# Kernel tuning notes

Hardware: AMD Instinct MI355X
Metric: run time of the kernel (lower is better)

Reference implementation:

```python
import jax, jax.numpy as jnp
import numpy as np

MARGIN = 0.2
LAMBDA_SOFTMAX = 9.0
LAMBDA_LSE = 6.0
WEIGHT_FACTOR = 0.7  # attn_prev is absent/zero on the i2t path
EPS = 1e-8
NEG_INF = -1e9


def setup_inputs() -> dict:
    key = jax.random.key(0)
    k1, k2, k3 = jax.random.split(key, 3)
    B, R, W, D = 128, 36, 32, 256  # batch, regions, max words, feat dim
    im = jax.random.normal(k1, (B, R, D), jnp.float32)
    s = jax.random.normal(k2, (B, W, D), jnp.float32)
    s_l = jax.random.randint(k3, (B,), 1, W + 1)  # caption lengths in [1, W]
    return {"im": im, "s": s, "s_l": s_l}


def _xattn_scores_i2t(im, s, s_l):
    # im: (B, R, D) images; s: (C, W, D) captions; s_l: (C,) lengths
    C, W = s.shape[0], s.shape[1]
    word_mask = jnp.arange(W)[None, :] < s_l[:, None]  # (C, W)

    # func_attention(query=images, context=caption words):
    # attn[c,b,w,r] = <s[c,w], im[b,r]>
    attn = jnp.einsum('cwd,brd->cbwr', s, im)
    # raw_feature_norm == 'clipped_l2norm': LeakyReLU(0.1) then l2norm over region axis
    attn = jax.nn.leaky_relu(attn, 0.1)
    attn = attn / (jnp.sqrt(jnp.sum(attn * attn, axis=-1, keepdims=True)) + EPS)
    # softmax over sourceL = words, with smoothing; mask padded words
    logits = jnp.where(word_mask[:, None, :, None], attn * LAMBDA_SOFTMAX, NEG_INF)
    A = jax.nn.softmax(logits, axis=2)  # (C, B, W, R), sums to 1 over words
    # weightedContext[c,b,r,:] = 0.7 * sum_w A[c,b,w,r] * s[c,w,:]
    wC = WEIGHT_FACTOR * jnp.einsum('cbwr,cwd->cbrd', A, s)

    # cosine similarity between image regions and weighted caption context
    num = jnp.sum(im[None] * wC, axis=-1)                      # (C, B, R)
    denom = jnp.linalg.norm(im, axis=-1)[None] * jnp.linalg.norm(wC, axis=-1)
    row_sim = num / jnp.clip(denom, EPS)

    # agg_func == 'LogSumExp' over regions
    sim = jax.nn.logsumexp(LAMBDA_LSE * row_sim, axis=2) / LAMBDA_LSE  # (C, B)
    return sim.T  # scores: (n_image, n_caption)


def reference(im, s, s_l):
    scores = _xattn_scores_i2t(im, s, s_l)
    diag = jnp.diag(scores)
    cost_s = jnp.clip(MARGIN + scores - diag[:, None], 0.0)   # caption retrieval
    cost_im = jnp.clip(MARGIN + scores - diag[None, :], 0.0)  # image retrieval
    eye = jnp.eye(scores.shape[0], dtype=bool)
    cost_s = jnp.where(eye, 0.0, cost_s)
    cost_im = jnp.where(eye, 0.0, cost_im)
    # max_violation=True: hardest negatives
    return jnp.sum(jnp.max(cost_s, axis=1)) + jnp.sum(jnp.max(cost_im, axis=0))
```

## Files before the change

### kernel.cpp

```cpp
#include <hip/hip_runtime.h>
#include <math.h>

#define CN 128
#define RN 36
#define WN 32
#define DN 256

#define SSTR  264
#define GSTR  40
#define ATSTR 40

#define WS_SCORES 0
#define WS_SF   65536
#define WS_IMF  (WS_SF + CN*16384)
#define WS_TAIL (WS_IMF + CN*16384)
#define WS_N2I  (WS_TAIL + CN*2048)
#define WS_NEED (WS_N2I + CN*RN*4)

typedef unsigned short u16;
typedef __attribute__((ext_vector_type(4))) unsigned short u16x4;
typedef __attribute__((ext_vector_type(8))) unsigned short u16x8;
typedef __attribute__((ext_vector_type(8))) __bf16 bf16x8;
typedef __attribute__((ext_vector_type(4))) float f32x4;

#define C9   12.9842502f
#define C6   8.65616798f
#define IC6  0.115524530f

__device__ __forceinline__ float bf2f(u16 u){ return __uint_as_float(((unsigned)u)<<16); }
__device__ __forceinline__ u16 f2bf(float f){ unsigned x=__float_as_uint(f); return (u16)((x + 0x7fffu + ((x>>16)&1u))>>16); }
__device__ __forceinline__ u16 f2bf_hw(float f){ __bf16 h = (__bf16)f; return __builtin_bit_cast(u16, h); }
__device__ __forceinline__ float lrelu(float v){ return fmaxf(v, 0.1f*v); }

__device__ __forceinline__ void gload16(const void* g, void* l){
    __builtin_amdgcn_global_load_lds((const __attribute__((address_space(1))) void*)g,
                                     (__attribute__((address_space(3))) void*)l, 16, 0, 0);
}

__global__ __launch_bounds__(256)
void precompute_kernel(const float* __restrict__ im, const float* __restrict__ s,
                       char* __restrict__ ws)
{
    const int tid = threadIdx.x;
    if (blockIdx.x < 128) {
        const int i = blockIdx.x;
        const float* src = s + (size_t)i*(WN*DN);
        u16* out = (u16*)(ws + WS_SF) + (size_t)i*8192;
#pragma unroll
        for (int it = 0; it < 4; it++) {
            int idx = tid + it*256;
            int m = idx >> 9, ks = (idx >> 6) & 7, ln = idx & 63;
            int col = ln & 15, g4 = ln >> 4;
            const float4* p = (const float4*)(src + (m*16+col)*DN + ks*32 + g4*8);
            float4 v0 = p[0], v1 = p[1];
            u16x8 hh = { f2bf_hw(v0.x),f2bf_hw(v0.y),f2bf_hw(v0.z),f2bf_hw(v0.w),
                         f2bf_hw(v1.x),f2bf_hw(v1.y),f2bf_hw(v1.z),f2bf_hw(v1.w) };
            *(u16x8*)(out + (size_t)idx*8) = hh;
        }
    } else {
        const int i = blockIdx.x - 128;
        const float* src = im + (size_t)i*(RN*DN);
        u16* out = (u16*)(ws + WS_IMF) + (size_t)i*8192;
#pragma unroll
        for (int it = 0; it < 4; it++) {
            int idx = tid + it*256;
            int m = idx >> 9, ks = (idx >> 6) & 7, ln = idx & 63;
            int col = ln & 15, g4 = ln >> 4;
            const float4* p = (const float4*)(src + (m*16+col)*DN + ks*32 + g4*8);
            float4 v0 = p[0], v1 = p[1];
            u16x8 hh = { f2bf_hw(v0.x),f2bf_hw(v0.y),f2bf_hw(v0.z),f2bf_hw(v0.w),
                         f2bf_hw(v1.x),f2bf_hw(v1.y),f2bf_hw(v1.z),f2bf_hw(v1.w) };
            *(u16x8*)(out + (size_t)idx*8) = hh;
        }
        if (tid < 128) {
            int row = tid >> 5, x = tid & 31;
            const float4* p = (const float4*)(src + (32+row)*DN + x*8);
            float4 v0 = p[0], v1 = p[1];
            u16x8 hh = { f2bf_hw(v0.x),f2bf_hw(v0.y),f2bf_hw(v0.z),f2bf_hw(v0.w),
                         f2bf_hw(v1.x),f2bf_hw(v1.y),f2bf_hw(v1.z),f2bf_hw(v1.w) };
            *(u16x8*)((u16*)(ws + WS_TAIL) + (size_t)i*1024 + row*256 + x*8) = hh;
        }
        float* n2o = (float*)(ws + WS_N2I) + (size_t)i*RN;
#pragma unroll
        for (int it = 0; it < 2; it++) {
            int idx = tid + it*256;
            if (idx < 288) {
                int r = idx >> 3, q = idx & 7;
                const float4* p = (const float4*)(src + r*DN + q*32);
                float ss = 0.f;
#pragma unroll
                for (int k = 0; k < 8; k++) {
                    float4 v = p[k];
                    ss = fmaf(v.x,v.x,ss); ss = fmaf(v.y,v.y,ss);
                    ss = fmaf(v.z,v.z,ss); ss = fmaf(v.w,v.w,ss);
                }
                ss += __shfl_xor(ss,1); ss += __shfl_xor(ss,2); ss += __shfl_xor(ss,4);
                if (q == 0) n2o[r] = ss;
            }
        }
    }
}

__global__ __launch_bounds__(512, 3)
void xattn_staged(const int* __restrict__ s_l, char* __restrict__ ws)
{
    __shared__ __align__(16) u16 smem[22016];
    u16* lds_g = smem + 4096;

    const int tid = threadIdx.x;
    const int lane = tid & 63, wv = tid >> 6;
    const int bq = blockIdx.x, cp = blockIdx.y;
    const int ci = wv >> 2, bi = wv & 3;
    const int c = cp*2 + ci, b = bq*4 + bi;
    const int col = lane & 15, g4 = lane >> 4;
    const int gm = bi >> 1, gn = bi & 1;
    const int L = s_l[c];
    const int r2c = (32+col > 35) ? 35 : 32+col;
    const int trow = (col > 3) ? 3 : col;

    {
        const char* tsrc = ws + WS_TAIL + (size_t)(bq*4)*2048;
        gload16(tsrc + wv*1024 + lane*16, (char*)smem + wv*1024);
    }
    const float* n2p = (const float*)(ws + WS_N2I) + (size_t)b*RN;
    float n2v0 = n2p[col];
    float n2v1 = n2p[16+col];
    float n2v2 = n2p[r2c];
    __syncthreads();

    const char* sf = ws + WS_SF  + (size_t)c*16384;
    const char* mf = ws + WS_IMF + (size_t)b*16384;
    const u16*  tl = smem + bi*1024;

    f32x4 raw[2][3];
#pragma unroll
    for (int m = 0; m < 2; m++)
#pragma unroll
        for (int n = 0; n < 3; n++) raw[m][n] = (f32x4){0.f,0.f,0.f,0.f};
    f32x4 gacc = {0.f,0.f,0.f,0.f};

#pragma unroll
    for (int ks = 0; ks < 8; ks++) {
        bf16x8 a0 = *(const bf16x8*)(sf +        ks*1024 + lane*16);
        bf16x8 a1 = *(const bf16x8*)(sf + 8192 + ks*1024 + lane*16);
        bf16x8 b0 = *(const bf16x8*)(mf +        ks*1024 + lane*16);
        bf16x8 b1 = *(const bf16x8*)(mf + 8192 + ks*1024 + lane*16);
        bf16x8 b2 = *(const bf16x8*)&tl[trow*256 + ks*32 + g4*8];
        bf16x8 ga = gm ? a1 : a0;
        bf16x8 gb = gn ? a1 : a0;
        raw[0][0] = __builtin_amdgcn_mfma_f32_16x16x32_bf16(a0, b0, raw[0][0], 0,0,0);
        raw[0][1] = __builtin_amdgcn_mfma_f32_16x16x32_bf16(a0, b1, raw[0][1], 0,0,0);
        raw[0][2] = __builtin_amdgcn_mfma_f32_16x16x32_bf16(a0, b2, raw[0][2], 0,0,0);
        raw[1][0] = __builtin_amdgcn_mfma_f32_16x16x32_bf16(a1, b0, raw[1][0], 0,0,0);
        raw[1][1] = __builtin_amdgcn_mfma_f32_16x16x32_bf16(a1, b1, raw[1][1], 0,0,0);
        raw[1][2] = __builtin_amdgcn_mfma_f32_16x16x32_bf16(a1, b2, raw[1][2], 0,0,0);
        gacc      = __builtin_amdgcn_mfma_f32_16x16x32_bf16(ga, gb, gacc, 0,0,0);
    }

    {
        u16x4 hg = { f2bf_hw(gacc[0]), f2bf_hw(gacc[1]), f2bf_hw(gacc[2]), f2bf_hw(gacc[3]) };
        *(u16x4*)&lds_g[ci*1280 + (gn*16+col)*GSTR + gm*16 + g4*4] = hg;
    }

    float af[2][3][4];
#pragma unroll
    for (int m = 0; m < 2; m++) {
#pragma unroll
        for (int reg = 0; reg < 4; reg++) {
            float ssum = 0.f;
#pragma unroll
            for (int n = 0; n < 3; n++) {
                float v = lrelu(raw[m][n][reg]);
                if (n == 2 && col >= 4) v = 0.f;
                af[m][n][reg] = v;
                ssum = fmaf(v, v, ssum);
            }
            ssum += __shfl_xor(ssum, 1);
            ssum += __shfl_xor(ssum, 2);
            ssum += __shfl_xor(ssum, 4);
            ssum += __shfl_xor(ssum, 8);
            float inv2 = C9 / (sqrtf(ssum) + 1e-8f);
#pragma unroll
            for (int n = 0; n < 3; n++) af[m][n][reg] *= inv2;
        }
    }

    float num[3];
#pragma unroll
    for (int n = 0; n < 3; n++) {
        float nm = 0.f;
#pragma unroll
        for (int m = 0; m < 2; m++)
#pragma unroll
            for (int reg = 0; reg < 4; reg++) {
                int w = m*16 + g4*4 + reg;
                float e = (w < L) ? __builtin_amdgcn_exp2f(af[m][n][reg]) : 0.f;
                af[m][n][reg] = e;
                nm = fmaf(e, raw[m][n][reg], nm);
            }
        nm += __shfl_xor(nm, 16);
        nm += __shfl_xor(nm, 32);
        num[n] = nm;
    }

    __syncthreads();

    u16* at = smem + 6656 + wv*1920;
#pragma unroll
    for (int m = 0; m < 2; m++)
#pragma unroll
        for (int n = 0; n < 3; n++) {
            u16x4 h = { f2bf_hw(af[m][n][0]), f2bf_hw(af[m][n][1]),
                        f2bf_hw(af[m][n][2]), f2bf_hw(af[m][n][3]) };
            *(u16x4*)&at[(n*16 + col)*ATSTR + m*16 + g4*4] = h;
        }

    bf16x8 gf0 = *(const bf16x8*)&lds_g[ci*1280 + col*GSTR + g4*8];
    bf16x8 gf1 = *(const bf16x8*)&lds_g[ci*1280 + (16+col)*GSTR + g4*8];

    float qv[3];
#pragma unroll
    for (int n = 0; n < 3; n++) {
        bf16x8 bfv = *(const bf16x8*)&at[(n*16 + col)*ATSTR + g4*8];
        f32x4 z = {0.f,0.f,0.f,0.f};
        f32x4 t0 = __builtin_amdgcn_mfma_f32_16x16x32_bf16(gf0, bfv, z, 0,0,0);
        f32x4 t1 = __builtin_amdgcn_mfma_f32_16x16x32_bf16(gf1, bfv, z, 0,0,0);
        float q = 0.f;
#pragma unroll
        for (int reg = 0; reg < 4; reg++) {
            q = fmaf(af[0][n][reg], t0[reg], q);
            q = fmaf(af[1][n][reg], t1[reg], q);
        }
        q += __shfl_xor(q, 16);
        q += __shfl_xor(q, 32);
        qv[n] = q;
    }

    float es = 0.f;
#pragma unroll
    for (int n = 0; n < 3; n++) {
        float n2a = (n == 0) ? n2v0 : (n == 1) ? n2v1 : n2v2;
        float rs = num[n] * rsqrtf(fmaxf(n2a * qv[n], 1e-16f));
        bool valid = (n < 2) || (col < 4);
        if (valid) es += __builtin_amdgcn_exp2f(C6 * rs);
    }
    es += __shfl_xor(es, 1);
    es += __shfl_xor(es, 2);
    es += __shfl_xor(es, 4);
    es += __shfl_xor(es, 8);

    if (lane == 0)
        ((float*)(ws + WS_SCORES))[(size_t)b * CN + c] =
            __builtin_amdgcn_logf(es) * IC6;
}

__global__ __launch_bounds__(512, 2)
void xattn_fallback(const float* __restrict__ im, const float* __restrict__ s,
                    const int* __restrict__ s_l, float* __restrict__ scores)
{
    __shared__ u16   s_lds[2][WN*SSTR];
    __shared__ u16   im_lds[4][RN*SSTR];
    __shared__ u16   g_lds[2][WN*GSTR];
    __shared__ u16   at_lds[8][48*ATSTR];
    __shared__ float n2i_lds[4][RN];

    const int tid  = threadIdx.x;
    const int lane = tid & 63;
    const int wv   = tid >> 6;
    const int bq   = blockIdx.x, cp = blockIdx.y;
    const int ci   = wv >> 2, bi = wv & 3;
    const int c    = cp*2 + ci, b = bq*4 + bi;
    const int col  = lane & 15, g4 = lane >> 4;

    if (wv < 4) {
        const float4* g = (const float4*)(im + (size_t)(bq*4 + wv) * (RN*DN));
        u16* dst = im_lds[wv];
#pragma unroll
        for (int k = 0; k < 36; k++) {
            int i = lane + k*64;
            float4 v = g[i];
            int row = i >> 6, cc = (i & 63) * 4;
            u16x4 h = { f2bf(v.x), f2bf(v.y), f2bf(v.z), f2bf(v.w) };
            *(u16x4*)&dst[row*SSTR + cc] = h;
        }
    } else {
        int cap = (wv - 4) >> 1;
        int l2  = ((wv - 4) & 1) * 64 + lane;
        const float4* g = (const float4*)(s + (size_t)(cp*2 + cap) * (WN*DN));
        u16* dst = s_lds[cap];
#pragma unroll
        for (int k = 0; k < 16; k++) {
            int i = l2 + k*128;
            float4 v = g[i];
            int row = i >> 6, cc = (i & 63) * 4;
            u16x4 h = { f2bf(v.x), f2bf(v.y), f2bf(v.z), f2bf(v.w) };
            *(u16x4*)&dst[row*SSTR + cc] = h;
        }
    }
    __syncthreads();

    {
        const int gm = (wv >> 1) & 1, gn = wv & 1;
        const u16* sb = s_lds[ci];
        f32x4 acc = {0.f, 0.f, 0.f, 0.f};
#pragma unroll
        for (int ks = 0; ks < 8; ks++) {
            int k0 = ks*32 + g4*8;
            bf16x8 af = *(const bf16x8*)&sb[(gm*16 + col)*SSTR + k0];
            bf16x8 bfv = *(const bf16x8*)&sb[(gn*16 + col)*SSTR + k0];
            acc = __builtin_amdgcn_mfma_f32_16x16x32_bf16(af, bfv, acc, 0, 0, 0);
        }
        u16x4 h = { f2bf(acc[0]), f2bf(acc[1]), f2bf(acc[2]), f2bf(acc[3]) };
        *(u16x4*)&g_lds[ci][(gn*16 + col)*GSTR + gm*16 + g4*4] = h;
    }

    if (wv < 4) {
        const u16* ib = im_lds[wv];
        int r = lane >> 1, half = lane & 1;
        float ss = 0.f;
        const u16x8* p = (const u16x8*)&ib[r*SSTR + half*128];
#pragma unroll
        for (int k = 0; k < 16; k++) {
            u16x8 v = p[k];
#pragma unroll
            for (int j = 0; j < 8; j++) { float f = bf2f(v[j]); ss = fmaf(f, f, ss); }
        }
        ss += __shfl_xor(ss, 1);
        if (half == 0) n2i_lds[wv][r] = ss;
        if (lane < 8) {
            int r2 = 32 + (lane >> 1), h2 = lane & 1;
            float s2 = 0.f;
            const u16x8* p2 = (const u16x8*)&ib[r2*SSTR + h2*128];
#pragma unroll
            for (int k = 0; k < 16; k++) {
                u16x8 v = p2[k];
#pragma unroll
                for (int j = 0; j < 8; j++) { float f = bf2f(v[j]); s2 = fmaf(f, f, s2); }
            }
            s2 += __shfl_xor(s2, 1);
            if (h2 == 0) n2i_lds[wv][r2] = s2;
        }
    }

    const u16* sb = s_lds[ci];
    const u16* ib = im_lds[bi];
    f32x4 raw[2][3];
#pragma unroll
    for (int m = 0; m < 2; m++)
#pragma unroll
        for (int n = 0; n < 3; n++) raw[m][n] = (f32x4){0.f,0.f,0.f,0.f};
    {
        int r2c = 32 + col; if (r2c > 35) r2c = 35;
#pragma unroll
        for (int ks = 0; ks < 8; ks++) {
            int k0 = ks*32 + g4*8;
            bf16x8 a0 = *(const bf16x8*)&sb[col*SSTR + k0];
            bf16x8 a1 = *(const bf16x8*)&sb[(16 + col)*SSTR + k0];
            bf16x8 b0 = *(const bf16x8*)&ib[col*SSTR + k0];
            bf16x8 b1 = *(const bf16x8*)&ib[(16 + col)*SSTR + k0];
            bf16x8 b2 = *(const bf16x8*)&ib[r2c*SSTR + k0];
            raw[0][0] = __builtin_amdgcn_mfma_f32_16x16x32_bf16(a0, b0, raw[0][0], 0,0,0);
            raw[0][1] = __builtin_amdgcn_mfma_f32_16x16x32_bf16(a0, b1, raw[0][1], 0,0,0);
            raw[0][2] = __builtin_amdgcn_mfma_f32_16x16x32_bf16(a0, b2, raw[0][2], 0,0,0);
            raw[1][0] = __builtin_amdgcn_mfma_f32_16x16x32_bf16(a1, b0, raw[1][0], 0,0,0);
            raw[1][1] = __builtin_amdgcn_mfma_f32_16x16x32_bf16(a1, b1, raw[1][1], 0,0,0);
            raw[1][2] = __builtin_amdgcn_mfma_f32_16x16x32_bf16(a1, b2, raw[1][2], 0,0,0);
        }
    }

    float af[2][3][4];
#pragma unroll
    for (int m = 0; m < 2; m++) {
#pragma unroll
        for (int reg = 0; reg < 4; reg++) {
            float ssum = 0.f;
#pragma unroll
            for (int n = 0; n < 3; n++) {
                float v = lrelu(raw[m][n][reg]);
                if (n == 2 && col >= 4) v = 0.f;
                af[m][n][reg] = v;
                ssum = fmaf(v, v, ssum);
            }
            ssum += __shfl_xor(ssum, 1);
            ssum += __shfl_xor(ssum, 2);
            ssum += __shfl_xor(ssum, 4);
            ssum += __shfl_xor(ssum, 8);
            float inv = 1.0f / (sqrtf(ssum) + 1e-8f);
#pragma unroll
            for (int n = 0; n < 3; n++) af[m][n][reg] *= inv;
        }
    }

    const int L = s_l[c];
    float num[3], qv[3];
#pragma unroll
    for (int n = 0; n < 3; n++) {
        float mx = -1e30f;
#pragma unroll
        for (int m = 0; m < 2; m++)
#pragma unroll
            for (int reg = 0; reg < 4; reg++) {
                int w = m*16 + g4*4 + reg;
                if (w < L) mx = fmaxf(mx, af[m][n][reg]);
            }
        mx = fmaxf(mx, __shfl_xor(mx, 16));
        mx = fmaxf(mx, __shfl_xor(mx, 32));
        mx *= 9.0f;
        float sme = 0.f;
#pragma unroll
        for (int m = 0; m < 2; m++)
#pragma unroll
            for (int reg = 0; reg < 4; reg++) {
                int w = m*16 + g4*4 + reg;
                float e = (w < L) ? __expf(fmaf(9.0f, af[m][n][reg], -mx)) : 0.f;
                af[m][n][reg] = e;
                sme += e;
            }
        sme += __shfl_xor(sme, 16);
        sme += __shfl_xor(sme, 32);
        float inv = 1.0f / sme;
        float nm = 0.f;
#pragma unroll
        for (int m = 0; m < 2; m++)
#pragma unroll
            for (int reg = 0; reg < 4; reg++) {
                af[m][n][reg] *= inv;
                nm = fmaf(af[m][n][reg], raw[m][n][reg], nm);
            }
        nm += __shfl_xor(nm, 16);
        nm += __shfl_xor(nm, 32);
        num[n] = nm;
    }

#pragma unroll
    for (int m = 0; m < 2; m++)
#pragma unroll
        for (int n = 0; n < 3; n++) {
            u16x4 h = { f2bf(af[m][n][0]), f2bf(af[m][n][1]),
                        f2bf(af[m][n][2]), f2bf(af[m][n][3]) };
            *(u16x4*)&at_lds[wv][(n*16 + col)*ATSTR + m*16 + g4*4] = h;
        }

    __syncthreads();

    bf16x8 gf0 = *(const bf16x8*)&g_lds[ci][col*GSTR + g4*8];
    bf16x8 gf1 = *(const bf16x8*)&g_lds[ci][(16+col)*GSTR + g4*8];
    f32x4 tt[2][3];
#pragma unroll
    for (int n = 0; n < 3; n++) {
        bf16x8 bfv = *(const bf16x8*)&at_lds[wv][(n*16 + col)*ATSTR + g4*8];
        f32x4 z = {0.f,0.f,0.f,0.f};
        tt[0][n] = __builtin_amdgcn_mfma_f32_16x16x32_bf16(gf0, bfv, z, 0,0,0);
        tt[1][n] = __builtin_amdgcn_mfma_f32_16x16x32_bf16(gf1, bfv, z, 0,0,0);
    }

#pragma unroll
    for (int n = 0; n < 3; n++) {
        float q = 0.f;
#pragma unroll
        for (int m = 0; m < 2; m++)
#pragma unroll
            for (int reg = 0; reg < 4; reg++) q = fmaf(af[m][n][reg], tt[m][n][reg], q);
        q += __shfl_xor(q, 16);
        q += __shfl_xor(q, 32);
        qv[n] = q;
    }

    float rs[3];
#pragma unroll
    for (int n = 0; n < 3; n++) {
        int r = n*16 + col; if (r > 35) r = 35;
        float n2 = n2i_lds[bi][r];
        float denom = fmaxf(0.7f * sqrtf(n2 * qv[n]), 1e-8f);
        rs[n] = 0.7f * num[n] / denom;
    }
    float xm = -1e30f;
#pragma unroll
    for (int n = 0; n < 3; n++) {
        bool valid = (n < 2) || (col < 4);
        if (valid) xm = fmaxf(xm, 6.0f * rs[n]);
    }
    xm = fmaxf(xm, __shfl_xor(xm, 1));
    xm = fmaxf(xm, __shfl_xor(xm, 2));
    xm = fmaxf(xm, __shfl_xor(xm, 4));
    xm = fmaxf(xm, __shfl_xor(xm, 8));
    float es = 0.f;
#pragma unroll
    for (int n = 0; n < 3; n++) {
        bool valid = (n < 2) || (col < 4);
        if (valid) es += __expf(6.0f * rs[n] - xm);
    }
    es += __shfl_xor(es, 1);
    es += __shfl_xor(es, 2);
    es += __shfl_xor(es, 4);
    es += __shfl_xor(es, 8);

    if (lane == 0) scores[(size_t)b * CN + c] = (xm + __logf(es)) / 6.0f;
}

__global__ __launch_bounds__(1024)
void contrastive_loss_kernel(const float* __restrict__ scores,
                             unsigned int* __restrict__ out)
{
    __shared__ float sc[128][129];
    __shared__ float dg[128];
    __shared__ float red[128];
    const int tid = threadIdx.x;

    const float4* s4 = (const float4*)scores;
#pragma unroll
    for (int it = 0; it < 4; it++) {
        int i = tid + it*1024;
        float4 v = s4[i];
        int row = i >> 5, c4 = (i & 31) << 2;
        sc[row][c4+0] = v.x; sc[row][c4+1] = v.y;
        sc[row][c4+2] = v.z; sc[row][c4+3] = v.w;
    }
    __syncthreads();
    if (tid < 128) dg[tid] = sc[tid][tid];
    __syncthreads();

    const int i = tid >> 3, g = tid & 7;
    const float di = dg[i];
    float rm = 0.f, cm = 0.f;
#pragma unroll
    for (int k = 0; k < 16; k++) {
        int j = g*16 + k;
        if (j != i) {
            rm = fmaxf(rm, 0.2f + sc[i][j] - di);
            cm = fmaxf(cm, 0.2f + sc[j][i] - di);
        }
    }
    rm = fmaxf(rm, __shfl_xor(rm, 1)); cm = fmaxf(cm, __shfl_xor(cm, 1));
    rm = fmaxf(rm, __shfl_xor(rm, 2)); cm = fmaxf(cm, __shfl_xor(cm, 2));
    rm = fmaxf(rm, __shfl_xor(rm, 4)); cm = fmaxf(cm, __shfl_xor(cm, 4));
    if (g == 0) red[i] = rm + cm;
    __syncthreads();

    if (tid < 64) {
        float v = red[tid] + red[tid + 64];
#pragma unroll
        for (int off = 32; off >= 1; off >>= 1) v += __shfl_xor(v, off);
        if (tid == 0) {
            unsigned int x = __float_as_uint(v);
            unsigned int h = (x + 0x7fffu + ((x >> 16) & 1u)) >> 16;
            out[0] = (h << 16) | h;
        }
    }
}

extern "C" void kernel_launch(void* const* d_in, const int* in_sizes, int n_in,
                              void* d_out, int out_size, void* d_ws, size_t ws_size,
                              hipStream_t stream) {
    const float* im  = (const float*)d_in[0];
    const float* s   = (const float*)d_in[1];
    const int*   s_l = (const int*)d_in[2];
    char* ws = (char*)d_ws;

    dim3 grid(32, 64);
    if (ws_size >= (size_t)WS_NEED) {
        precompute_kernel<<<256, 256, 0, stream>>>(im, s, ws);
        xattn_staged<<<grid, 512, 0, stream>>>(s_l, ws);
    } else {
        xattn_fallback<<<grid, 512, 0, stream>>>(im, s, s_l, (float*)ws);
    }
    contrastive_loss_kernel<<<1, 1024, 0, stream>>>((const float*)ws, (unsigned int*)d_out);
}
```

Before: 48.85 us.

## Precompute caption Gram matrices and tail fragments, removing block syncs in main kernel

The per-caption Gram matrix (s·sᵀ in bf16) is now computed once per caption in the precompute kernel and stored to workspace, instead of being recomputed by every wave in the main kernel. The image tail rows are also pre-laid out in MFMA fragment order so the main kernel loads them directly from global memory rather than staging them through LDS. This drops both __syncthreads barriers and shrinks main-kernel LDS, which could raise occupancy, at the cost of extra global reads per wave and a heavier precompute kernel.

New measurement: 46.37 us. -5.1%, faster.

```diff
diff --git a/kernel.cpp b/kernel.cpp
--- a/kernel.cpp
+++ b/kernel.cpp
@@ -11,11 +11,12 @@
 #define ATSTR 40
 
 #define WS_SCORES 0
-#define WS_SF   65536
-#define WS_IMF  (WS_SF + CN*16384)
-#define WS_TAIL (WS_IMF + CN*16384)
-#define WS_N2I  (WS_TAIL + CN*2048)
-#define WS_NEED (WS_N2I + CN*RN*4)
+#define WS_SF    65536
+#define WS_IMF   (WS_SF + CN*16384)
+#define WS_TAILF (WS_IMF + CN*16384)
+#define WS_G     (WS_TAILF + CN*8192)
+#define WS_N2I   (WS_G + CN*2048)
+#define WS_NEED  (WS_N2I + CN*RN*4)
 
 typedef unsigned short u16;
 typedef __attribute__((ext_vector_type(4))) unsigned short u16x4;
@@ -44,41 +45,72 @@
     const int tid = threadIdx.x;
     if (blockIdx.x < 128) {
         const int i = blockIdx.x;
+        __shared__ __align__(16) u16 s_lds[WN*SSTR];
+        __shared__ __align__(16) u16 g_lds[WN*GSTR];
         const float* src = s + (size_t)i*(WN*DN);
-        u16* out = (u16*)(ws + WS_SF) + (size_t)i*8192;
+        u16* outf = (u16*)(ws + WS_SF) + (size_t)i*8192;
 #pragma unroll
         for (int it = 0; it < 4; it++) {
             int idx = tid + it*256;
             int m = idx >> 9, ks = (idx >> 6) & 7, ln = idx & 63;
-            int col = ln & 15, g4 = ln >> 4;
-            const float4* p = (const float4*)(src + (m*16+col)*DN + ks*32 + g4*8);
+            int cc = ln & 15, gg = ln >> 4;
+            const float4* p = (const float4*)(src + (m*16+cc)*DN + ks*32 + gg*8);
             float4 v0 = p[0], v1 = p[1];
             u16x8 hh = { f2bf_hw(v0.x),f2bf_hw(v0.y),f2bf_hw(v0.z),f2bf_hw(v0.w),
                          f2bf_hw(v1.x),f2bf_hw(v1.y),f2bf_hw(v1.z),f2bf_hw(v1.w) };
-            *(u16x8*)(out + (size_t)idx*8) = hh;
+            *(u16x8*)(outf + (size_t)idx*8) = hh;
+            *(u16x8*)&s_lds[(m*16+cc)*SSTR + ks*32 + gg*8] = hh;
+        }
+        __syncthreads();
+        {
+            const int lane = tid & 63, wv = tid >> 6;
+            const int cc = lane & 15, gg = lane >> 4;
+            const int gm = wv >> 1, gn = wv & 1;
+            f32x4 acc = {0.f,0.f,0.f,0.f};
+#pragma unroll
+            for (int ks = 0; ks < 8; ks++) {
+                int k0 = ks*32 + gg*8;
+                bf16x8 a  = *(const bf16x8*)&s_lds[(gm*16+cc)*SSTR + k0];
+                bf16x8 bb = *(const bf16x8*)&s_lds[(gn*16+cc)*SSTR + k0];
+                acc = __builtin_amdgcn_mfma_f32_16x16x32_bf16(a, bb, acc, 0, 0, 0);
+            }
+            u16x4 hg = { f2bf_hw(acc[0]), f2bf_hw(acc[1]), f2bf_hw(acc[2]), f2bf_hw(acc[3]) };
+            *(u16x4*)&g_lds[(gn*16+cc)*GSTR + gm*16 + gg*4] = hg;
+        }
+        __syncthreads();
+        if (tid < 128) {
+            int t = tid >> 6, ln = tid & 63;
+            int cc = ln & 15, gg = ln >> 4;
+            u16x8 gv = *(const u16x8*)&g_lds[(t*16+cc)*GSTR + gg*8];
+            *(u16x8*)((u16*)(ws + WS_G) + (size_t)i*1024 + tid*8) = gv;
         }
     } else {
         const int i = blockIdx.x - 128;
         const float* src = im + (size_t)i*(RN*DN);
-        u16* out = (u16*)(ws + WS_IMF) + (size_t)i*8192;
+        u16* outf = (u16*)(ws + WS_IMF) + (size_t)i*8192;
 #pragma unroll
         for (int it = 0; it < 4; it++) {
             int idx = tid + it*256;
             int m = idx >> 9, ks = (idx >> 6) & 7, ln = idx & 63;
-            int col = ln & 15, g4 = ln >> 4;
-            const float4* p = (const float4*)(src + (m*16+col)*DN + ks*32 + g4*8);
+            int cc = ln & 15, gg = ln >> 4;
+            const float4* p = (const float4*)(src + (m*16+cc)*DN + ks*32 + gg*8);
             float4 v0 = p[0], v1 = p[1];
             u16x8 hh = { f2bf_hw(v0.x),f2bf_hw(v0.y),f2bf_hw(v0.z),f2bf_hw(v0.w),
                          f2bf_hw(v1.x),f2bf_hw(v1.y),f2bf_hw(v1.z),f2bf_hw(v1.w) };
-            *(u16x8*)(out + (size_t)idx*8) = hh;
-        }
-        if (tid < 128) {
-            int row = tid >> 5, x = tid & 31;
-            const float4* p = (const float4*)(src + (32+row)*DN + x*8);
+            *(u16x8*)(outf + (size_t)idx*8) = hh;
+        }
+        u16* tout = (u16*)(ws + WS_TAILF) + (size_t)i*4096;
+#pragma unroll
+        for (int it = 0; it < 2; it++) {
+            int idx = tid + it*256;
+            int ks = idx >> 6, ln = idx & 63;
+            int cc = ln & 15, gg = ln >> 4;
+            int trow = (cc > 3) ? 3 : cc;
+            const float4* p = (const float4*)(src + (32+trow)*DN + ks*32 + gg*8);
             float4 v0 = p[0], v1 = p[1];
             u16x8 hh = { f2bf_hw(v0.x),f2bf_hw(v0.y),f2bf_hw(v0.z),f2bf_hw(v0.w),
                          f2bf_hw(v1.x),f2bf_hw(v1.y),f2bf_hw(v1.z),f2bf_hw(v1.w) };
-            *(u16x8*)((u16*)(ws + WS_TAIL) + (size_t)i*1024 + row*256 + x*8) = hh;
+            *(u16x8*)(tout + (size_t)idx*8) = hh;
         }
         float* n2o = (float*)(ws + WS_N2I) + (size_t)i*RN;
 #pragma unroll
@@ -104,8 +136,7 @@
 __global__ __launch_bounds__(512, 3)
 void xattn_staged(const int* __restrict__ s_l, char* __restrict__ ws)
 {
-    __shared__ __align__(16) u16 smem[22016];
-    u16* lds_g = smem + 4096;
+    __shared__ __align__(16) u16 at_all[8*48*ATSTR];
 
     const int tid = threadIdx.x;
     const int lane = tid & 63, wv = tid >> 6;
@@ -113,31 +144,26 @@
     const int ci = wv >> 2, bi = wv & 3;
     const int c = cp*2 + ci, b = bq*4 + bi;
     const int col = lane & 15, g4 = lane >> 4;
-    const int gm = bi >> 1, gn = bi & 1;
     const int L = s_l[c];
     const int r2c = (32+col > 35) ? 35 : 32+col;
-    const int trow = (col > 3) ? 3 : col;
-
-    {
-        const char* tsrc = ws + WS_TAIL + (size_t)(bq*4)*2048;
-        gload16(tsrc + wv*1024 + lane*16, (char*)smem + wv*1024);
-    }
+
+    const char* sf  = ws + WS_SF    + (size_t)c*16384;
+    const char* mf  = ws + WS_IMF   + (size_t)b*16384;
+    const char* tf  = ws + WS_TAILF + (size_t)b*8192;
+    const char* gfp = ws + WS_G     + (size_t)c*2048;
+
+    bf16x8 gf0 = *(const bf16x8*)(gfp + lane*16);
+    bf16x8 gf1 = *(const bf16x8*)(gfp + 1024 + lane*16);
     const float* n2p = (const float*)(ws + WS_N2I) + (size_t)b*RN;
     float n2v0 = n2p[col];
     float n2v1 = n2p[16+col];
     float n2v2 = n2p[r2c];
-    __syncthreads();
-
-    const char* sf = ws + WS_SF  + (size_t)c*16384;
-    const char* mf = ws + WS_IMF + (size_t)b*16384;
-    const u16*  tl = smem + bi*1024;
 
     f32x4 raw[2][3];
 #pragma unroll
     for (int m = 0; m < 2; m++)
 #pragma unroll
         for (int n = 0; n < 3; n++) raw[m][n] = (f32x4){0.f,0.f,0.f,0.f};
-    f32x4 gacc = {0.f,0.f,0.f,0.f};
 
 #pragma unroll
     for (int ks = 0; ks < 8; ks++) {
@@ -145,21 +171,13 @@
         bf16x8 a1 = *(const bf16x8*)(sf + 8192 + ks*1024 + lane*16);
         bf16x8 b0 = *(const bf16x8*)(mf +        ks*1024 + lane*16);
         bf16x8 b1 = *(const bf16x8*)(mf + 8192 + ks*1024 + lane*16);
-        bf16x8 b2 = *(const bf16x8*)&tl[trow*256 + ks*32 + g4*8];
-        bf16x8 ga = gm ? a1 : a0;
-        bf16x8 gb = gn ? a1 : a0;
+        bf16x8 b2 = *(const bf16x8*)(tf +        ks*1024 + lane*16);
         raw[0][0] = __builtin_amdgcn_mfma_f32_16x16x32_bf16(a0, b0, raw[0][0], 0,0,0);
         raw[0][1] = __builtin_amdgcn_mfma_f32_16x16x32_bf16(a0, b1, raw[0][1], 0,0,0);
         raw[0][2] = __builtin_amdgcn_mfma_f32_16x16x32_bf16(a0, b2, raw[0][2], 0,0,0);
         raw[1][0] = __builtin_amdgcn_mfma_f32_16x16x32_bf16(a1, b0, raw[1][0], 0,0,0);
         raw[1][1] = __builtin_amdgcn_mfma_f32_16x16x32_bf16(a1, b1, raw[1][1], 0,0,0);
         raw[1][2] = __builtin_amdgcn_mfma_f32_16x16x32_bf16(a1, b2, raw[1][2], 0,0,0);
-        gacc      = __builtin_amdgcn_mfma_f32_16x16x32_bf16(ga, gb, gacc, 0,0,0);
-    }
-
-    {
-        u16x4 hg = { f2bf_hw(gacc[0]), f2bf_hw(gacc[1]), f2bf_hw(gacc[2]), f2bf_hw(gacc[3]) };
-        *(u16x4*)&lds_g[ci*1280 + (gn*16+col)*GSTR + gm*16 + g4*4] = hg;
     }
 
     float af[2][3][4];
@@ -203,9 +221,7 @@
         num[n] = nm;
     }
 
-    __syncthreads();
-
-    u16* at = smem + 6656 + wv*1920;
+    u16* at = at_all + wv*1920;
 #pragma unroll
     for (int m = 0; m < 2; m++)
 #pragma unroll
@@ -214,9 +230,6 @@
                         f2bf_hw(af[m][n][2]), f2bf_hw(af[m][n][3]) };
             *(u16x4*)&at[(n*16 + col)*ATSTR + m*16 + g4*4] = h;
         }
-
-    bf16x8 gf0 = *(const bf16x8*)&lds_g[ci*1280 + col*GSTR + g4*8];
-    bf16x8 gf1 = *(const bf16x8*)&lds_g[ci*1280 + (16+col)*GSTR + g4*8];
 
     float qv[3];
 #pragma unroll
```
